# Performance work log

Measured on AMD Instinct MI355X. Metric: run time of the kernel, lower is better.

## Reference

```python
import jax, jax.numpy as jnp
import numpy as np

B, N, D, H = 4, 2048, 1024, 16
HD = D // H


def setup_inputs() -> dict:
    key = jax.random.key(0)
    ks = jax.random.split(key, 9)
    s = 1.0 / np.sqrt(D)
    return {
        "x": jax.random.normal(ks[0], (B, N, D), jnp.float32),
        "Wq": jax.random.normal(ks[1], (D, D), jnp.float32) * s,
        "bq": jnp.zeros((D,), jnp.float32),
        "Wk": jax.random.normal(ks[2], (D, D), jnp.float32) * s,
        "bk": jnp.zeros((D,), jnp.float32),
        "Wv": jax.random.normal(ks[3], (D, D), jnp.float32) * s,
        "bv": jnp.zeros((D,), jnp.float32),
        "Wo": jax.random.normal(ks[4], (D, D), jnp.float32) * s,
        "bo": jnp.zeros((D,), jnp.float32),
    }


def reference(x, Wq, bq, Wk, bk, Wv, bv, Wo, bo):
    Bx, Nx, Dx = x.shape
    q = x @ Wq + bq  # [B,N,D]
    k = x @ Wk + bk
    v = x @ Wv + bv
    # split heads -> [B,H,N,hd]
    q = q.reshape(Bx, Nx, H, HD).transpose(0, 2, 1, 3)
    k = k.reshape(Bx, Nx, H, HD).transpose(0, 2, 1, 3)
    v = v.reshape(Bx, Nx, H, HD).transpose(0, 2, 1, 3)
    q = q / jnp.sqrt(jnp.asarray(HD, q.dtype))
    scores = jnp.einsum("bhqd,bhkd->bhqk", q, k)
    # causal mask: additive -1e9 strictly above diagonal (matches torch.triu diag=1)
    mask = jnp.triu(jnp.full((Nx, Nx), -1e9, dtype=scores.dtype), k=1)
    probs = jax.nn.softmax(scores + mask, axis=-1)
    out = jnp.einsum("bhqk,bhkd->bhqd", probs, v)  # [B,H,N,hd]
    out = out.transpose(0, 2, 1, 3).reshape(Bx, Nx, Dx)  # concat heads
    return out @ Wo + bo
```

## Files before the change

### kernel.cpp

```cpp
#include <hip/hip_runtime.h>
#include <hip/hip_bf16.h>


#define BB 4
#define NN 2048
#define DD 1024
#define HH 16
#define HD 64
#define MM (BB * NN)

typedef __bf16 bf16;
typedef __bf16 bf16x8 __attribute__((ext_vector_type(8)));
typedef float f32x4 __attribute__((ext_vector_type(4)));

__device__ __forceinline__ void async_copy16(bf16* lds, const bf16* g) {
    __builtin_amdgcn_global_load_lds(
        (const __attribute__((address_space(1))) void*)g,
        (__attribute__((address_space(3))) void*)lds, 16, 0, 0);
}

__global__ void convert_x(const float* __restrict__ x, bf16* __restrict__ xb) {
    int i = (blockIdx.x * 256 + threadIdx.x) * 4;
    float4 v = *(const float4*)&x[i];
    xb[i + 0] = (bf16)v.x;
    xb[i + 1] = (bf16)v.y;
    xb[i + 2] = (bf16)v.z;
    xb[i + 3] = (bf16)v.w;
}

__global__ void transpose_w4(const float* __restrict__ W0, const float* __restrict__ W1,
                             const float* __restrict__ W2, const float* __restrict__ W3,
                             bf16* __restrict__ Wt) {
    __shared__ float tile[32][33];
    const float* W = (blockIdx.z == 0) ? W0 : (blockIdx.z == 1) ? W1
                    : (blockIdx.z == 2) ? W2 : W3;
    bf16* out = Wt + (size_t)blockIdx.z * DD * DD;
    int tx = threadIdx.x, ty = threadIdx.y;
    int x0 = blockIdx.x * 32, y0 = blockIdx.y * 32;
#pragma unroll
    for (int i = 0; i < 32; i += 8)
        tile[ty + i][tx] = W[(size_t)(y0 + ty + i) * DD + x0 + tx];
    __syncthreads();
#pragma unroll
    for (int i = 0; i < 32; i += 8)
        out[(size_t)(x0 + ty + i) * DD + y0 + tx] = (bf16)tile[tx][ty + i];
}

template <int MODE>
__global__ __launch_bounds__(256) void gemm_bt(
    const bf16* __restrict__ A, const bf16* __restrict__ Wt,
    const float* __restrict__ b0, const float* __restrict__ b1,
    const float* __restrict__ b2, void* __restrict__ out0,
    void* __restrict__ out1, void* __restrict__ out2) {
    const int K = DD;
    __shared__ __align__(16) bf16 As[128 * 32];
    __shared__ __align__(16) bf16 Bs[128 * 32];
    __shared__ __align__(16) bf16 Cs[MODE == 0 ? 128 * 136 : 1];

    int m0 = blockIdx.x * 128;
    int n0 = blockIdx.y * 128;

    const bf16* Wz;
    const float* bias;
    void* out;
    float scale = 1.0f;
    int z = 0;
    if (MODE == 0) {
        z = blockIdx.z;
        Wz = Wt + (size_t)z * DD * DD;
        bias = (z == 0) ? b0 : ((z == 1) ? b1 : b2);
        out = (z == 0) ? out0 : ((z == 1) ? out1 : out2);
        if (z == 0) scale = 0.125f * 1.44269504f;
    } else {
        Wz = Wt; bias = b0; out = out0;
    }

    int tid = threadIdx.x;
    int w = tid >> 6, lane = tid & 63;
    int wm = w >> 1, wn = w & 1;
    int quad = lane >> 4, l16 = lane & 15;

    f32x4 acc[4][4];
#pragma unroll
    for (int i = 0; i < 4; i++)
#pragma unroll
        for (int j = 0; j < 4; j++) acc[i][j] = (f32x4){0.f, 0.f, 0.f, 0.f};

    for (int k0 = 0; k0 < K; k0 += 32) {
        __syncthreads();
#pragma unroll
        for (int j = 0; j < 2; j++) {
            int c = j * 256 + w * 64 + lane;
            int row = c >> 2, kk = (c & 3) * 8;
            async_copy16(&As[c * 8], &A[(size_t)(m0 + row) * K + k0 + kk]);
            async_copy16(&Bs[c * 8], &Wz[(size_t)(n0 + row) * K + k0 + kk]);
        }
        __syncthreads();

        bf16x8 af[4], bfm[4];
#pragma unroll
        for (int i = 0; i < 4; i++) {
            af[i] = *(const bf16x8*)&As[(wm * 64 + i * 16 + l16) * 32 + quad * 8];
            bfm[i] = *(const bf16x8*)&Bs[(wn * 64 + i * 16 + l16) * 32 + quad * 8];
        }
#pragma unroll
        for (int i = 0; i < 4; i++)
#pragma unroll
            for (int j = 0; j < 4; j++)
                acc[i][j] = __builtin_amdgcn_mfma_f32_16x16x32_bf16(
                    af[i], bfm[j], acc[i][j], 0, 0, 0);
    }

    if (MODE == 0) {
#pragma unroll
        for (int j = 0; j < 4; j++) {
            int nl = wn * 64 + j * 16 + l16;
            float bv = bias[n0 + nl];
#pragma unroll
            for (int i = 0; i < 4; i++) {
#pragma unroll
                for (int r = 0; r < 4; r++) {
                    int ml = wm * 64 + i * 16 + quad * 4 + r;
                    bf16 v = (bf16)((acc[i][j][r] + bv) * scale);
                    if (z == 2) Cs[nl * 136 + ml] = v;
                    else        Cs[ml * 136 + nl] = v;
                }
            }
        }
        __syncthreads();

        int bidx = m0 >> 11;
        int tok0 = m0 & (NN - 1);
        int hh0 = n0 >> 6;
        if (z != 2) {
#pragma unroll
            for (int hf = 0; hf < 2; hf++) {
                bf16* base = (bf16*)out + ((size_t)(bidx * HH + hh0 + hf) * NN + tok0) * HD;
#pragma unroll
                for (int k = 0; k < 4; k++) {
                    int f = k * 2048 + tid * 8;
                    int tok = f >> 6, hd = f & 63;
                    *(bf16x8*)&base[f] = *(const bf16x8*)&Cs[tok * 136 + hf * 64 + hd];
                }
            }
        } else {
#pragma unroll
            for (int hf = 0; hf < 2; hf++) {
#pragma unroll
                for (int k = 0; k < 4; k++) {
                    int hd = k * 16 + (tid >> 4);
                    int tk = (tid & 15) * 8;
                    bf16* dst = (bf16*)out +
                        ((size_t)(bidx * HH + hh0 + hf) * HD + hd) * NN + tok0 + tk;
                    *(bf16x8*)dst = *(const bf16x8*)&Cs[(hf * 64 + hd) * 136 + tk];
                }
            }
        }
    } else {
#pragma unroll
        for (int j = 0; j < 4; j++) {
            int n = n0 + wn * 64 + j * 16 + l16;
            float bv = bias[n];
#pragma unroll
            for (int i = 0; i < 4; i++) {
                int mrow = m0 + wm * 64 + i * 16 + quad * 4;
#pragma unroll
                for (int r = 0; r < 4; r++)
                    ((float*)out)[(size_t)(mrow + r) * DD + n] = acc[i][j][r] + bv;
            }
        }
    }
}

__global__ __launch_bounds__(256) void flash_attn(
    const bf16* __restrict__ Q, const bf16* __restrict__ Kg,
    const bf16* __restrict__ Vt_g, bf16* __restrict__ Oc) {
    __shared__ __align__(16) bf16 Ks[128 * 72];
    __shared__ __align__(16) bf16 Vs[64 * 136];
    __shared__ __align__(16) bf16 Ps[128 * 136];

    int bh = blockIdx.y;
    int b = bh >> 4, h = bh & 15;
    int tid = threadIdx.x;
    int w = tid >> 6, lane = tid & 63;
    int quad = lane >> 4, l16 = lane & 15;

    const bf16* Qb = Q + (size_t)bh * NN * HD;
    const bf16* Kb = Kg + (size_t)bh * NN * HD;
    const bf16* Vtb = Vt_g + (size_t)bh * HD * NN;

    bf16x8 ones;
#pragma unroll
    for (int i = 0; i < 8; i++) ones[i] = (bf16)1.0f;

    for (int phase = 0; phase < 2; phase++) {
        int qi = (phase == 0) ? blockIdx.x : (15 - blockIdx.x);
        int q0 = qi * 128;

        bf16x8 qf[2][2];
#pragma unroll
        for (int mi = 0; mi < 2; mi++)
#pragma unroll
            for (int ks = 0; ks < 2; ks++)
                qf[mi][ks] = *(const bf16x8*)&Qb[(size_t)(q0 + w * 32 + mi * 16 + l16) * HD +
                                                ks * 32 + quad * 8];

        f32x4 l_sum[2];
        f32x4 o_acc[2][4];
#pragma unroll
        for (int mi = 0; mi < 2; mi++) {
            l_sum[mi] = (f32x4){0.f, 0.f, 0.f, 0.f};
#pragma unroll
            for (int di = 0; di < 4; di++) o_acc[mi][di] = (f32x4){0.f, 0.f, 0.f, 0.f};
        }

        int wave_qmax = q0 + w * 32 + 31;
        int kv_end = q0 + 128;

        for (int kv0 = 0; kv0 < kv_end; kv0 += 128) {
            __syncthreads();

#pragma unroll
            for (int j = 0; j < 4; j++) {
                int c = j * 256 + tid;
                int r = c >> 3, c8 = (c & 7) * 8;
                *(bf16x8*)&Ks[r * 72 + c8] = *(const bf16x8*)&Kb[(size_t)(kv0 + r) * HD + c8];
            }
#pragma unroll
            for (int j = 0; j < 4; j++) {
                int c = j * 256 + tid;
                int d = c >> 4, k8 = (c & 15) * 8;
                *(bf16x8*)&Vs[d * 136 + k8] = *(const bf16x8*)&Vtb[(size_t)d * NN + kv0 + k8];
            }
            __syncthreads();

            if (kv0 <= wave_qmax) {
#pragma unroll
                for (int ni = 0; ni < 8; ni++) {
                    bf16x8 bk0 = *(const bf16x8*)&Ks[(ni * 16 + l16) * 72 + quad * 8];
                    bf16x8 bk1 = *(const bf16x8*)&Ks[(ni * 16 + l16) * 72 + 32 + quad * 8];
                    f32x4 s0 = (f32x4){0.f, 0.f, 0.f, 0.f};
                    f32x4 s1 = (f32x4){0.f, 0.f, 0.f, 0.f};
                    s0 = __builtin_amdgcn_mfma_f32_16x16x32_bf16(qf[0][0], bk0, s0, 0, 0, 0);
                    s0 = __builtin_amdgcn_mfma_f32_16x16x32_bf16(qf[0][1], bk1, s0, 0, 0, 0);
                    s1 = __builtin_amdgcn_mfma_f32_16x16x32_bf16(qf[1][0], bk0, s1, 0, 0, 0);
                    s1 = __builtin_amdgcn_mfma_f32_16x16x32_bf16(qf[1][1], bk1, s1, 0, 0, 0);
                    int col = kv0 + ni * 16 + l16;
#pragma unroll
                    for (int r = 0; r < 4; r++) {
                        int row0 = q0 + w * 32 + quad * 4 + r;
                        float p0 = (col > row0) ? 0.f : exp2f(s0[r]);
                        float p1 = (col > row0 + 16) ? 0.f : exp2f(s1[r]);
                        Ps[(w * 32 + quad * 4 + r) * 136 + ni * 16 + l16] = (bf16)p0;
                        Ps[(w * 32 + 16 + quad * 4 + r) * 136 + ni * 16 + l16] = (bf16)p1;
                    }
                }

#pragma unroll
                for (int ks = 0; ks < 4; ks++) {
                    bf16x8 pf0 = *(const bf16x8*)&Ps[(w * 32 + l16) * 136 + ks * 32 + quad * 8];
                    bf16x8 pf1 = *(const bf16x8*)&Ps[(w * 32 + 16 + l16) * 136 + ks * 32 + quad * 8];
                    l_sum[0] = __builtin_amdgcn_mfma_f32_16x16x32_bf16(pf0, ones, l_sum[0], 0, 0, 0);
                    l_sum[1] = __builtin_amdgcn_mfma_f32_16x16x32_bf16(pf1, ones, l_sum[1], 0, 0, 0);
#pragma unroll
                    for (int di = 0; di < 4; di++) {
                        bf16x8 bv = *(const bf16x8*)&Vs[(di * 16 + l16) * 136 + ks * 32 + quad * 8];
                        o_acc[0][di] = __builtin_amdgcn_mfma_f32_16x16x32_bf16(pf0, bv, o_acc[0][di], 0, 0, 0);
                        o_acc[1][di] = __builtin_amdgcn_mfma_f32_16x16x32_bf16(pf1, bv, o_acc[1][di], 0, 0, 0);
                    }
                }
            }
        }

#pragma unroll
        for (int mi = 0; mi < 2; mi++)
#pragma unroll
            for (int r = 0; r < 4; r++) {
                float inv = 1.0f / l_sum[mi][r];
                int tok = q0 + w * 32 + mi * 16 + quad * 4 + r;
#pragma unroll
                for (int di = 0; di < 4; di++) {
                    int d = h * 64 + di * 16 + l16;
                    Oc[((size_t)(b * NN + tok)) * DD + d] = (bf16)(o_acc[mi][di][r] * inv);
                }
            }
    }
}

extern "C" void kernel_launch(void* const* d_in, const int* in_sizes, int n_in,
                              void* d_out, int out_size, void* d_ws, size_t ws_size,
                              hipStream_t stream) {
    const float* x  = (const float*)d_in[0];
    const float* Wq = (const float*)d_in[1];
    const float* bq = (const float*)d_in[2];
    const float* Wk = (const float*)d_in[3];
    const float* bk = (const float*)d_in[4];
    const float* Wv = (const float*)d_in[5];
    const float* bv = (const float*)d_in[6];
    const float* Wo = (const float*)d_in[7];
    const float* bo = (const float*)d_in[8];

    const size_t need = (size_t)(8388608ull * 5 + 4194304ull) * sizeof(bf16);
    if (ws_size < need) return;

    bf16* ws = (bf16*)d_ws;
    bf16* xb = ws;
    bf16* wt = xb + (size_t)MM * DD;
    bf16* Qw = wt + 4ull * DD * DD;
    bf16* Kw = Qw + (size_t)MM * DD;
    bf16* Vw = Kw + (size_t)MM * DD;
    bf16* Aw = Vw + (size_t)MM * DD;

    convert_x<<<dim3(MM * DD / 1024), 256, 0, stream>>>(x, xb);

    transpose_w4<<<dim3(32, 32, 4), dim3(32, 8), 0, stream>>>(Wq, Wk, Wv, Wo, wt);

    gemm_bt<0><<<dim3(MM / 128, DD / 128, 3), 256, 0, stream>>>(
        xb, wt, bq, bk, bv, Qw, Kw, Vw);

    flash_attn<<<dim3(8, BB * HH), 256, 0, stream>>>(Qw, Kw, Vw, Aw);

    gemm_bt<1><<<dim3(MM / 128, DD / 128, 1), 256, 0, stream>>>(
        Aw, wt + 3ull * DD * DD, bo, bo, bo, d_out, d_out, d_out);
}
```

Baseline: 281.0 us.

## Share K/V tile loads across paired query blocks in causal flash attention

Each block processes its two paired query tiles (qi and 15-qi) together in a single KV loop, so each K/V tile is loaded into LDS once and reused for both query tiles. Before, the two tiles ran in sequential phases and reloaded the same K/V prefix. Masking is split into a templated unmasked path for full tiles and a masked path for diagonal tiles only, which drops the per-element compare on most tiles. In exchange, register pressure roughly doubles because two sets of Q fragments and accumulators are live at once, which may lower occupancy or cause spills.

```diff
diff --git a/kernel.cpp b/kernel.cpp
--- a/kernel.cpp
+++ b/kernel.cpp
@@ -172,6 +172,50 @@
     }
 }
 
+template <bool MASKED>
+__device__ __forceinline__ void fa_compute(
+    const bf16* Ks, const bf16* Vs, bf16* Ps,
+    const bf16x8 qf[2][2], f32x4 l_sum[2], f32x4 o_acc[2][4],
+    int w, int quad, int l16, const bf16x8& ones) {
+#pragma unroll
+    for (int ni = 0; ni < 8; ni++) {
+        bf16x8 bk0 = *(const bf16x8*)&Ks[(ni * 16 + l16) * 72 + quad * 8];
+        bf16x8 bk1 = *(const bf16x8*)&Ks[(ni * 16 + l16) * 72 + 32 + quad * 8];
+        f32x4 s0 = (f32x4){0.f, 0.f, 0.f, 0.f};
+        f32x4 s1 = (f32x4){0.f, 0.f, 0.f, 0.f};
+        s0 = __builtin_amdgcn_mfma_f32_16x16x32_bf16(qf[0][0], bk0, s0, 0, 0, 0);
+        s0 = __builtin_amdgcn_mfma_f32_16x16x32_bf16(qf[0][1], bk1, s0, 0, 0, 0);
+        s1 = __builtin_amdgcn_mfma_f32_16x16x32_bf16(qf[1][0], bk0, s1, 0, 0, 0);
+        s1 = __builtin_amdgcn_mfma_f32_16x16x32_bf16(qf[1][1], bk1, s1, 0, 0, 0);
+#pragma unroll
+        for (int r = 0; r < 4; r++) {
+            float p0 = exp2f(s0[r]);
+            float p1 = exp2f(s1[r]);
+            if (MASKED) {
+                int col = ni * 16 + l16;
+                int row0 = w * 32 + quad * 4 + r;
+                if (col > row0) p0 = 0.f;
+                if (col > row0 + 16) p1 = 0.f;
+            }
+            Ps[(w * 32 + quad * 4 + r) * 136 + ni * 16 + l16] = (bf16)p0;
+            Ps[(w * 32 + 16 + quad * 4 + r) * 136 + ni * 16 + l16] = (bf16)p1;
+        }
+    }
+#pragma unroll
+    for (int ks = 0; ks < 4; ks++) {
+        bf16x8 pf0 = *(const bf16x8*)&Ps[(w * 32 + l16) * 136 + ks * 32 + quad * 8];
+        bf16x8 pf1 = *(const bf16x8*)&Ps[(w * 32 + 16 + l16) * 136 + ks * 32 + quad * 8];
+        l_sum[0] = __builtin_amdgcn_mfma_f32_16x16x32_bf16(pf0, ones, l_sum[0], 0, 0, 0);
+        l_sum[1] = __builtin_amdgcn_mfma_f32_16x16x32_bf16(pf1, ones, l_sum[1], 0, 0, 0);
+#pragma unroll
+        for (int di = 0; di < 4; di++) {
+            bf16x8 bv = *(const bf16x8*)&Vs[(di * 16 + l16) * 136 + ks * 32 + quad * 8];
+            o_acc[0][di] = __builtin_amdgcn_mfma_f32_16x16x32_bf16(pf0, bv, o_acc[0][di], 0, 0, 0);
+            o_acc[1][di] = __builtin_amdgcn_mfma_f32_16x16x32_bf16(pf1, bv, o_acc[1][di], 0, 0, 0);
+        }
+    }
+}
+
 __global__ __launch_bounds__(256) void flash_attn(
     const bf16* __restrict__ Q, const bf16* __restrict__ Kg,
     const bf16* __restrict__ Vt_g, bf16* __restrict__ Oc) {
@@ -193,98 +237,78 @@
 #pragma unroll
     for (int i = 0; i < 8; i++) ones[i] = (bf16)1.0f;
 
-    for (int phase = 0; phase < 2; phase++) {
-        int qi = (phase == 0) ? blockIdx.x : (15 - blockIdx.x);
-        int q0 = qi * 128;
-
-        bf16x8 qf[2][2];
-#pragma unroll
-        for (int mi = 0; mi < 2; mi++)
-#pragma unroll
-            for (int ks = 0; ks < 2; ks++)
-                qf[mi][ks] = *(const bf16x8*)&Qb[(size_t)(q0 + w * 32 + mi * 16 + l16) * HD +
-                                                ks * 32 + quad * 8];
-
-        f32x4 l_sum[2];
-        f32x4 o_acc[2][4];
-#pragma unroll
-        for (int mi = 0; mi < 2; mi++) {
-            l_sum[mi] = (f32x4){0.f, 0.f, 0.f, 0.f};
-#pragma unroll
-            for (int di = 0; di < 4; di++) o_acc[mi][di] = (f32x4){0.f, 0.f, 0.f, 0.f};
-        }
-
-        int wave_qmax = q0 + w * 32 + 31;
-        int kv_end = q0 + 128;
-
-        for (int kv0 = 0; kv0 < kv_end; kv0 += 128) {
-            __syncthreads();
-
-#pragma unroll
-            for (int j = 0; j < 4; j++) {
-                int c = j * 256 + tid;
-                int r = c >> 3, c8 = (c & 7) * 8;
-                *(bf16x8*)&Ks[r * 72 + c8] = *(const bf16x8*)&Kb[(size_t)(kv0 + r) * HD + c8];
-            }
-#pragma unroll
-            for (int j = 0; j < 4; j++) {
-                int c = j * 256 + tid;
-                int d = c >> 4, k8 = (c & 15) * 8;
-                *(bf16x8*)&Vs[d * 136 + k8] = *(const bf16x8*)&Vtb[(size_t)d * NN + kv0 + k8];
-            }
-            __syncthreads();
-
-            if (kv0 <= wave_qmax) {
-#pragma unroll
-                for (int ni = 0; ni < 8; ni++) {
-                    bf16x8 bk0 = *(const bf16x8*)&Ks[(ni * 16 + l16) * 72 + quad * 8];
-                    bf16x8 bk1 = *(const bf16x8*)&Ks[(ni * 16 + l16) * 72 + 32 + quad * 8];
-                    f32x4 s0 = (f32x4){0.f, 0.f, 0.f, 0.f};
-                    f32x4 s1 = (f32x4){0.f, 0.f, 0.f, 0.f};
-                    s0 = __builtin_amdgcn_mfma_f32_16x16x32_bf16(qf[0][0], bk0, s0, 0, 0, 0);
-                    s0 = __builtin_amdgcn_mfma_f32_16x16x32_bf16(qf[0][1], bk1, s0, 0, 0, 0);
-                    s1 = __builtin_amdgcn_mfma_f32_16x16x32_bf16(qf[1][0], bk0, s1, 0, 0, 0);
-                    s1 = __builtin_amdgcn_mfma_f32_16x16x32_bf16(qf[1][1], bk1, s1, 0, 0, 0);
-                    int col = kv0 + ni * 16 + l16;
-#pragma unroll
-                    for (int r = 0; r < 4; r++) {
-                        int row0 = q0 + w * 32 + quad * 4 + r;
-                        float p0 = (col > row0) ? 0.f : exp2f(s0[r]);
-                        float p1 = (col > row0 + 16) ? 0.f : exp2f(s1[r]);
-                        Ps[(w * 32 + quad * 4 + r) * 136 + ni * 16 + l16] = (bf16)p0;
-                        Ps[(w * 32 + 16 + quad * 4 + r) * 136 + ni * 16 + l16] = (bf16)p1;
-                    }
-                }
-
-#pragma unroll
-                for (int ks = 0; ks < 4; ks++) {
-                    bf16x8 pf0 = *(const bf16x8*)&Ps[(w * 32 + l16) * 136 + ks * 32 + quad * 8];
-                    bf16x8 pf1 = *(const bf16x8*)&Ps[(w * 32 + 16 + l16) * 136 + ks * 32 + quad * 8];
-                    l_sum[0] = __builtin_amdgcn_mfma_f32_16x16x32_bf16(pf0, ones, l_sum[0], 0, 0, 0);
-                    l_sum[1] = __builtin_amdgcn_mfma_f32_16x16x32_bf16(pf1, ones, l_sum[1], 0, 0, 0);
-#pragma unroll
-                    for (int di = 0; di < 4; di++) {
-                        bf16x8 bv = *(const bf16x8*)&Vs[(di * 16 + l16) * 136 + ks * 32 + quad * 8];
-                        o_acc[0][di] = __builtin_amdgcn_mfma_f32_16x16x32_bf16(pf0, bv, o_acc[0][di], 0, 0, 0);
-                        o_acc[1][di] = __builtin_amdgcn_mfma_f32_16x16x32_bf16(pf1, bv, o_acc[1][di], 0, 0, 0);
-                    }
-                }
-            }
-        }
-
-#pragma unroll
-        for (int mi = 0; mi < 2; mi++)
-#pragma unroll
-            for (int r = 0; r < 4; r++) {
-                float inv = 1.0f / l_sum[mi][r];
-                int tok = q0 + w * 32 + mi * 16 + quad * 4 + r;
-#pragma unroll
-                for (int di = 0; di < 4; di++) {
-                    int d = h * 64 + di * 16 + l16;
-                    Oc[((size_t)(b * NN + tok)) * DD + d] = (bf16)(o_acc[mi][di][r] * inv);
-                }
-            }
-    }
+    int qiA = blockIdx.x;
+    int qiB = 15 - qiA;
+    int q0A = qiA * 128, q0B = qiB * 128;
+
+    bf16x8 qfA[2][2], qfB[2][2];
+#pragma unroll
+    for (int mi = 0; mi < 2; mi++)
+#pragma unroll
+        for (int ks = 0; ks < 2; ks++) {
+            qfA[mi][ks] = *(const bf16x8*)&Qb[(size_t)(q0A + w * 32 + mi * 16 + l16) * HD +
+                                             ks * 32 + quad * 8];
+            qfB[mi][ks] = *(const bf16x8*)&Qb[(size_t)(q0B + w * 32 + mi * 16 + l16) * HD +
+                                             ks * 32 + quad * 8];
+        }
+
+    f32x4 l_sumA[2], l_sumB[2];
+    f32x4 o_accA[2][4], o_accB[2][4];
+#pragma unroll
+    for (int mi = 0; mi < 2; mi++) {
+        l_sumA[mi] = (f32x4){0.f, 0.f, 0.f, 0.f};
+        l_sumB[mi] = (f32x4){0.f, 0.f, 0.f, 0.f};
+#pragma unroll
+        for (int di = 0; di < 4; di++) {
+            o_accA[mi][di] = (f32x4){0.f, 0.f, 0.f, 0.f};
+            o_accB[mi][di] = (f32x4){0.f, 0.f, 0.f, 0.f};
+        }
+    }
+
+    for (int t = 0; t <= qiB; t++) {
+        int kv0 = t * 128;
+        __syncthreads();
+
+#pragma unroll
+        for (int j = 0; j < 4; j++) {
+            int c = j * 256 + tid;
+            int r = c >> 3, c8 = (c & 7) * 8;
+            *(bf16x8*)&Ks[r * 72 + c8] = *(const bf16x8*)&Kb[(size_t)(kv0 + r) * HD + c8];
+        }
+#pragma unroll
+        for (int j = 0; j < 4; j++) {
+            int c = j * 256 + tid;
+            int d = c >> 4, k8 = (c & 15) * 8;
+            *(bf16x8*)&Vs[d * 136 + k8] = *(const bf16x8*)&Vtb[(size_t)d * NN + kv0 + k8];
+        }
+        __syncthreads();
+
+        if (t < qiA)
+            fa_compute<false>(Ks, Vs, Ps, qfA, l_sumA, o_accA, w, quad, l16, ones);
+        else if (t == qiA)
+            fa_compute<true>(Ks, Vs, Ps, qfA, l_sumA, o_accA, w, quad, l16, ones);
+
+        if (t < qiB)
+            fa_compute<false>(Ks, Vs, Ps, qfB, l_sumB, o_accB, w, quad, l16, ones);
+        else
+            fa_compute<true>(Ks, Vs, Ps, qfB, l_sumB, o_accB, w, quad, l16, ones);
+    }
+
+#pragma unroll
+    for (int mi = 0; mi < 2; mi++)
+#pragma unroll
+        for (int r = 0; r < 4; r++) {
+            float invA = 1.0f / l_sumA[mi][r];
+            float invB = 1.0f / l_sumB[mi][r];
+            int tokA = q0A + w * 32 + mi * 16 + quad * 4 + r;
+            int tokB = q0B + w * 32 + mi * 16 + quad * 4 + r;
+#pragma unroll
+            for (int di = 0; di < 4; di++) {
+                int d = h * 64 + di * 16 + l16;
+                Oc[((size_t)(b * NN + tokA)) * DD + d] = (bf16)(o_accA[mi][di][r] * invA);
+                Oc[((size_t)(b * NN + tokB)) * DD + d] = (bf16)(o_accB[mi][di][r] * invB);
+            }
+        }
 }
 
 extern "C" void kernel_launch(void* const* d_in, const int* in_sizes, int n_in,
```

New measurement: 363.1 us. 1.29x slower.
